# Kernel tuning notes

Hardware: AMD Instinct MI355X
Metric: run time of the kernel (lower is better)

## Reference

```python
import jax, jax.numpy as jnp
import numpy as np

N = 100000          # nodes
E = 3200000         # edges (before self-loops)
F_IN = 500          # Pubmed feature dim
H1, C1 = 8, 8       # layer-1 heads, channels per head
H2, C2 = 1, 7       # layer-2 heads, channels (num classes)
NEG_SLOPE = 0.2


def _glorot(key, shape, fan_in):
    return jax.random.normal(key, shape, dtype=jnp.float32) / np.sqrt(fan_in)


def setup_inputs() -> dict:
    key = jax.random.key(0)
    ks = jax.random.split(key, 10)
    x = jax.random.normal(ks[0], (N, F_IN), dtype=jnp.float32)
    edge_index = jax.random.randint(ks[1], (2, E), 0, N, dtype=jnp.int64)
    W1 = _glorot(ks[2], (F_IN, H1 * C1), F_IN)
    a_src1 = _glorot(ks[3], (H1, C1), C1)
    a_dst1 = _glorot(ks[4], (H1, C1), C1)
    b1 = jnp.zeros((H1 * C1,), dtype=jnp.float32)
    W2 = _glorot(ks[5], (H1 * C1, H2 * C2), H1 * C1)
    a_src2 = _glorot(ks[6], (H2, C2), C2)
    a_dst2 = _glorot(ks[7], (H2, C2), C2)
    b2 = jnp.zeros((H2 * C2,), dtype=jnp.float32)
    return {"x": x, "edge_index": edge_index, "W1": W1, "a_src1": a_src1,
            "a_dst1": a_dst1, "b1": b1, "W2": W2, "a_src2": a_src2,
            "a_dst2": a_dst2, "b2": b2}


def gat_conv(x, src, dst, W, a_src, a_dst, bias, heads, out_ch):
    # x: [N, F_in]; src/dst: [E'] (self-loops included); returns [N, heads*out_ch]
    h = (x @ W).reshape(N, heads, out_ch)                      # [N, H, C]
    alpha_s = jnp.einsum('nhc,hc->nh', h, a_src)               # [N, H]
    alpha_d = jnp.einsum('nhc,hc->nh', h, a_dst)               # [N, H]
    e = alpha_s[src] + alpha_d[dst]                            # [E', H]
    e = jax.nn.leaky_relu(e, NEG_SLOPE)
    # segment softmax over incoming edges of each dst node
    m = jax.ops.segment_max(e, dst, num_segments=N)            # [N, H]
    ex = jnp.exp(e - m[dst])                                   # [E', H]
    denom = jax.ops.segment_sum(ex, dst, num_segments=N)       # [N, H]
    alpha = ex / denom[dst]                                    # [E', H]
    msg = alpha[:, :, None] * h[src]                           # [E', H, C]
    out = jax.ops.segment_sum(msg, dst, num_segments=N)        # [N, H, C]
    return out.reshape(N, heads * out_ch) + bias


def reference(x, edge_index, W1, a_src1, a_dst1, b1, W2, a_src2, a_dst2, b2):
    loops = jnp.arange(N, dtype=edge_index.dtype)
    src = jnp.concatenate([edge_index[0], loops])
    dst = jnp.concatenate([edge_index[1], loops])
    h = gat_conv(x, src, dst, W1, a_src1, a_dst1, b1, H1, C1)   # [N, 64]
    out = gat_conv(h, src, dst, W2, a_src2, a_dst2, b2, H2, C2) # [N, 7]
    return jax.nn.log_softmax(out, axis=1)
```

## Files before the change

kernel.cpp:

```cpp
#include <hip/hip_runtime.h>
#include <hip/hip_bf16.h>
#include <hip/hip_fp16.h>

#define N_NODES 100000
#define N_EDGES 3200000
#define ET (N_EDGES + N_NODES)
#define F_IN 500
#define H1 8
#define C1 8
#define F1 64
#define C2 7

#define BSH 6
#define NB ((N_NODES + 63) / 64)
#define CAP2 4096
#define FB 128
#define FCHUNK ((ET + FB - 1) / FB)

typedef __attribute__((ext_vector_type(8))) short short8;
typedef __attribute__((ext_vector_type(4))) float f32x4;

__device__ __forceinline__ unsigned short f2bf(float f) {
    const unsigned u = __float_as_uint(f);
    return (unsigned short)((u + 0x7FFFu + ((u >> 16) & 1u)) >> 16);
}

__global__ __launch_bounds__(1024) void fill_count(const int* __restrict__ ei,
                                                   int* __restrict__ cntmat) {
    __shared__ int hist[NB];
    const int t = threadIdx.x, blk = blockIdx.x;
    for (int i = t; i < NB; i += 1024) hist[i] = 0;
    __syncthreads();
    const int s0 = blk * FCHUNK;
    const int s1 = min(s0 + FCHUNK, ET);
    for (int i = s0 + t; i < s1; i += 1024) {
        const int dst = (i < N_EDGES) ? ei[N_EDGES + i] : (i - N_EDGES);
        atomicAdd(&hist[dst >> BSH], 1);
    }
    __syncthreads();
    int* row = cntmat + (size_t)blk * NB;
    for (int i = t; i < NB; i += 1024) row[i] = hist[i];
}

__global__ __launch_bounds__(1024) void scan2a(const int* __restrict__ cntmat,
                                               int* __restrict__ boff,
                                               int* __restrict__ bexcl) {
    __shared__ int tot[2048];
    __shared__ int wsum[16];
    const int t = threadIdx.x;
    const int lane = t & 63;
    const int w = t >> 6;
    for (int b = t; b < 2048; b += 1024) {
        int s = 0;
        if (b < NB)
            for (int j = 0; j < FB; ++j) s += cntmat[(size_t)j * NB + b];
        tot[b] = s;
    }
    __syncthreads();
    int running = 0;
    for (int t0 = 0; t0 < 2048; t0 += 1024) {
        const int v = tot[t0 + t];
        int sc = v;
#pragma unroll
        for (int d = 1; d < 64; d <<= 1) {
            int u = __shfl_up(sc, d);
            if (lane >= d) sc += u;
        }
        if (lane == 63) wsum[w] = sc;
        __syncthreads();
        if (t < 16) {
            int ws = wsum[t];
#pragma unroll
            for (int d = 1; d < 16; d <<= 1) {
                int u = __shfl_up(ws, d);
                if (t >= d) ws += u;
            }
            wsum[t] = ws;
        }
        __syncthreads();
        const int excl = running + (w ? wsum[w - 1] : 0) + sc - v;
        if (t0 + t < NB) {
            boff[t0 + t] = excl;
            bexcl[t0 + t] = excl;
        }
        const int tt = wsum[15];
        __syncthreads();
        running += tt;
    }
    if (t == 0) boff[NB] = running;
}

__global__ __launch_bounds__(256) void scan2b(const int* __restrict__ cntmat,
                                              const int* __restrict__ bexcl,
                                              int* __restrict__ basemat) {
    const int b = blockIdx.x * 256 + threadIdx.x;
    if (b >= NB) return;
    int run = bexcl[b];
#pragma unroll 4
    for (int j = 0; j < FB; ++j) {
        basemat[(size_t)j * NB + b] = run;
        run += cntmat[(size_t)j * NB + b];
    }
}

__global__ __launch_bounds__(1024) void fill_scatter(const int* __restrict__ ei,
                                                     const int* __restrict__ basemat,
                                                     unsigned int* __restrict__ ebuf) {
    __shared__ int cur[NB];
    const int t = threadIdx.x, blk = blockIdx.x;
    const int* row = basemat + (size_t)blk * NB;
    for (int i = t; i < NB; i += 1024) cur[i] = row[i];
    __syncthreads();
    const int s0 = blk * FCHUNK;
    const int s1 = min(s0 + FCHUNK, ET);
    for (int i = s0 + t; i < s1; i += 1024) {
        int src, dst;
        if (i < N_EDGES) { src = ei[i]; dst = ei[N_EDGES + i]; }
        else             { src = dst = i - N_EDGES; }
        const int b = dst >> BSH;
        const int p = atomicAdd(&cur[b], 1);
        ebuf[p] = (unsigned)src | ((unsigned)(dst & 63) << 17);
    }
}

__global__ __launch_bounds__(256) void wprep(const float* __restrict__ W1,
                                             short* __restrict__ wpk) {
    const int idx = blockIdx.x * 256 + threadIdx.x;
    if (idx >= 32768) return;
    const int j = idx & 7;
    const int l = (idx >> 3) & 63;
    const int f = (idx >> 9) & 3;
    const int ks = idx >> 11;
    const int k = ks * 32 + ((l >> 4) << 3) + j;
    const int col = f * 16 + (l & 15);
    const float fv = (k < F_IN) ? W1[k * F1 + col] : 0.f;
    wpk[idx] = (short)f2bf(fv);
}

__global__ __launch_bounds__(256) void gemm1_kernel(
    const float* __restrict__ x, const short* __restrict__ wpk,
    const float* __restrict__ a_src, const float* __restrict__ a_dst,
    __half* __restrict__ h1, float* __restrict__ as1, float* __restrict__ ad1)
{
    const int t = threadIdx.x;
    const int l = t & 63;
    const int w = t >> 6;
    const int row0 = blockIdx.x * 64 + w * 16;
    const int r = l & 15;
    const int koff = (l >> 4) * 8;
    const float* __restrict__ xp =
        x + (size_t)min(row0 + r, N_NODES - 1) * F_IN + koff;
    const short* __restrict__ wl = wpk + (l << 3);

    f32x4 acc[4];
#pragma unroll
    for (int f = 0; f < 4; ++f) acc[f] = (f32x4){0.f, 0.f, 0.f, 0.f};

    float4 va = *(const float4*)(xp);
    float4 vb = *(const float4*)(xp + 4);
    short8 bcur[4];
#pragma unroll
    for (int f = 0; f < 4; ++f)
        bcur[f] = *(const short8*)(wl + (f << 9));

    for (int ks = 0; ks < 16; ++ks) {
        float v[8];
        v[0] = va.x; v[1] = va.y; v[2] = va.z; v[3] = va.w;
        v[4] = vb.x; v[5] = vb.y; v[6] = vb.z; v[7] = vb.w;
        if (ks < 14) {
            va = *(const float4*)(xp + (ks + 1) * 32);
            vb = *(const float4*)(xp + (ks + 1) * 32 + 4);
        } else if (ks == 14) {
            float tv[8];
#pragma unroll
            for (int j = 0; j < 8; ++j)
                tv[j] = (koff + j < 20) ? xp[480 + j] : 0.f;
            va = make_float4(tv[0], tv[1], tv[2], tv[3]);
            vb = make_float4(tv[4], tv[5], tv[6], tv[7]);
        }
        short8 bnext[4];
        if (ks < 15) {
#pragma unroll
            for (int f = 0; f < 4; ++f)
                bnext[f] = *(const short8*)(wl + (((ks + 1) * 4 + f) << 9));
        }
        short8 ah, al;
#pragma unroll
        for (int j = 0; j < 8; ++j) {
            const unsigned short h = f2bf(v[j]);
            ah[j] = (short)h;
            al[j] = (short)f2bf(v[j] - __uint_as_float((unsigned)h << 16));
        }
#pragma unroll
        for (int f = 0; f < 4; ++f) {
            acc[f] = __builtin_amdgcn_mfma_f32_16x16x32_bf16(ah, bcur[f], acc[f], 0, 0, 0);
            acc[f] = __builtin_amdgcn_mfma_f32_16x16x32_bf16(al, bcur[f], acc[f], 0, 0, 0);
        }
        if (ks < 15) {
#pragma unroll
            for (int f = 0; f < 4; ++f) bcur[f] = bnext[f];
        }
    }

    const int g = l >> 4;
    const int p = r >> 3;
    float asv[4], adv[4];
#pragma unroll
    for (int f = 0; f < 4; ++f) {
        asv[f] = a_src[f * 16 + r];
        adv[f] = a_dst[f * 16 + r];
    }
#pragma unroll
    for (int f = 0; f < 4; ++f) {
#pragma unroll
        for (int reg = 0; reg < 4; ++reg) {
            const int row = row0 + g * 4 + reg;
            const float hv = acc[f][reg];
            if (row < N_NODES)
                h1[(size_t)row * F1 + f * 16 + r] = __float2half(hv);
            float ps = hv * asv[f];
            float pd = hv * adv[f];
            ps += __shfl_xor(ps, 1); ps += __shfl_xor(ps, 2); ps += __shfl_xor(ps, 4);
            pd += __shfl_xor(pd, 1); pd += __shfl_xor(pd, 2); pd += __shfl_xor(pd, 4);
            if ((l & 7) == 0 && row < N_NODES) {
                as1[row * H1 + f * 2 + p] = ps;
                ad1[row * H1 + f * 2 + p] = pd;
            }
        }
    }
}

__global__ __launch_bounds__(256) void agg1_kernel(
    const int* __restrict__ boff, const unsigned int* __restrict__ ebuf,
    const __half* __restrict__ h1, const float* __restrict__ as1,
    const float* __restrict__ ad1, const float* __restrict__ b1,
    __half* __restrict__ hout, int* __restrict__ colidx,
    int* __restrict__ rowptrg)
{
    __shared__ int colb[CAP2];
    __shared__ int hist[64], curs[64], rowp[65];
    const int t = threadIdx.x, b = blockIdx.x;
    const int e0 = boff[b];
    const int cnt = boff[b + 1] - e0;
    const int l = t & 63;
    const int w = t >> 6;
    if (t < 64) hist[t] = 0;
    __syncthreads();

    if (cnt <= CAP2) {
        for (int i = t; i < cnt; i += 256)
            atomicAdd(&hist[ebuf[e0 + i] >> 17], 1);
        __syncthreads();
        if (t < 64) {
            const int v = hist[t];
            int sc = v;
#pragma unroll
            for (int d = 1; d < 64; d <<= 1) {
                int u = __shfl_up(sc, d);
                if (t >= d) sc += u;
            }
            rowp[t] = sc - v;
            curs[t] = sc - v;
            if (t == 63) rowp[64] = sc;
        }
        __syncthreads();
        for (int i = t; i < cnt; i += 256) {
            const unsigned v = ebuf[e0 + i];
            const int p = atomicAdd(&curs[v >> 17], 1);
            colb[p] = (int)(v & 0x1FFFFu);
        }
        __syncthreads();
        for (int i = t; i < cnt; i += 256) colidx[e0 + i] = colb[i];
        if (t < 65) rowptrg[b * 65 + t] = e0 + rowp[t];

        const int jsub = l & 7;
        const int hsub = l >> 3;
        const int pbase = l & 56;
        for (int ni = 0; ni < 16; ++ni) {
            const int d = w * 16 + ni;
            const int n = (b << 6) + d;
            if (n >= N_NODES) break;
            const int rr0 = rowp[d], rr1 = rowp[d + 1];
            const float adh = ad1[(n << 3) + hsub];
            float den = 0.f, acc = 0.f;
            int j0 = rr0;
            for (; j0 + 8 <= rr1; j0 += 8) {
                const int s_l = colb[j0 + jsub];
                float e = as1[(s_l << 3) + hsub] + adh;
                e = fmaxf(e, 0.2f * e);
                const float p_l = __expf(e);
#pragma unroll
                for (int j = 0; j < 8; ++j) {
                    const float p = __shfl(p_l, pbase + j);
                    const int s_j = __builtin_amdgcn_readlane(s_l, j);
                    const float v = __half2float(h1[((size_t)(unsigned)s_j << 6) + l]);
                    den += p;
                    acc = fmaf(p, v, acc);
                }
            }
            if (j0 < rr1) {
                const int s_l = colb[min(j0 + jsub, rr1 - 1)];
                float e = as1[(s_l << 3) + hsub] + adh;
                e = fmaxf(e, 0.2f * e);
                const float p_l = __expf(e);
#pragma unroll
                for (int j = 0; j < 8; ++j) {
                    if (j0 + j < rr1) {
                        const float p = __shfl(p_l, pbase + j);
                        const int s_j = __builtin_amdgcn_readlane(s_l, j);
                        const float v = __half2float(h1[((size_t)(unsigned)s_j << 6) + l]);
                        den += p;
                        acc = fmaf(p, v, acc);
                    }
                }
            }
            hout[((size_t)n << 6) + l] = __float2half(acc / den + b1[l]);
        }
    } else {
        const int hsub = l >> 3;
        for (int ni = 0; ni < 16; ++ni) {
            const int d = w * 16 + ni;
            const int n = (b << 6) + d;
            if (n >= N_NODES) break;
            const float adh = ad1[(n << 3) + hsub];
            float den = 0.f, acc = 0.f;
            for (int i = 0; i < cnt; ++i) {
                const unsigned v = ebuf[e0 + i];
                if ((int)(v >> 17) == d) {
                    const int s = (int)(v & 0x1FFFFu);
                    float e = as1[(s << 3) + hsub] + adh;
                    e = fmaxf(e, 0.2f * e);
                    const float p = __expf(e);
                    const float hv = __half2float(h1[((size_t)s << 6) + l]);
                    den += p;
                    acc = fmaf(p, hv, acc);
                }
            }
            hout[((size_t)n << 6) + l] = __float2half(acc / den + b1[l]);
        }
    }
}

__global__ __launch_bounds__(256) void gemm2_kernel(
    const __half* __restrict__ hin, const float* __restrict__ W2,
    const float* __restrict__ a_src, const float* __restrict__ a_dst,
    float* __restrict__ h2p, float* __restrict__ as2, float* __restrict__ ad2)
{
    __shared__ float w2s[F1 * C2];
    __shared__ float as_s[C2], ad_s[C2];
    for (int i = threadIdx.x; i < F1 * C2; i += blockDim.x) w2s[i] = W2[i];
    if (threadIdx.x < C2) { as_s[threadIdx.x] = a_src[threadIdx.x]; ad_s[threadIdx.x] = a_dst[threadIdx.x]; }
    __syncthreads();

    int n = blockIdx.x * blockDim.x + threadIdx.x;
    if (n >= N_NODES) return;
    float acc[C2];
#pragma unroll
    for (int c = 0; c < C2; ++c) acc[c] = 0.f;
    const short8* hp = (const short8*)(hin + ((size_t)n << 6));
#pragma unroll
    for (int k8 = 0; k8 < 8; ++k8) {
        const short8 h8 = hp[k8];
#pragma unroll
        for (int e = 0; e < 8; ++e) {
            const float hv = __half2float(__ushort_as_half((unsigned short)h8[e]));
            const int k = k8 * 8 + e;
#pragma unroll
            for (int c = 0; c < C2; ++c)
                acc[c] = fmaf(hv, w2s[k * C2 + c], acc[c]);
        }
    }
    float s = 0.f, d = 0.f;
#pragma unroll
    for (int c = 0; c < C2; ++c) {
        s = fmaf(acc[c], as_s[c], s);
        d = fmaf(acc[c], ad_s[c], d);
    }
    float4* o = (float4*)(h2p + (size_t)n * 8);
    o[0] = make_float4(acc[0], acc[1], acc[2], acc[3]);
    o[1] = make_float4(acc[4], acc[5], acc[6], 0.f);
    as2[n] = s;
    ad2[n] = d;
}

__global__ __launch_bounds__(256) void agg2_kernel(
    const int* __restrict__ boff, const unsigned int* __restrict__ ebuf,
    const int* __restrict__ rowptrg, const int* __restrict__ colidx,
    const float* __restrict__ h2p, const float* __restrict__ as2,
    const float* __restrict__ ad2, const float* __restrict__ b2,
    float* __restrict__ out)
{
    const int t = threadIdx.x, b = blockIdx.x;
    const int d = t >> 2;
    const int q = t & 3;
    const int n = (b << 6) + d;
    if (n >= N_NODES) return;
    const int cnt = boff[b + 1] - boff[b];
    const float adn = ad2[n];

    float denom = 0.f;
    float a0 = 0, a1 = 0, a2 = 0, a3 = 0, a4 = 0, a5 = 0, a6 = 0;
    if (cnt <= CAP2) {
        const int rr0 = rowptrg[b * 65 + d], rr1 = rowptrg[b * 65 + d + 1];
        for (int j = rr0 + q; j < rr1; j += 4) {
            const int s = colidx[j];
            float e = as2[s] + adn;
            e = fmaxf(e, 0.2f * e);
            const float ex = __expf(e);
            const float4 va = *(const float4*)(h2p + (size_t)s * 8);
            const float4 vb = *(const float4*)(h2p + (size_t)s * 8 + 4);
            denom += ex;
            a0 = fmaf(ex, va.x, a0); a1 = fmaf(ex, va.y, a1);
            a2 = fmaf(ex, va.z, a2); a3 = fmaf(ex, va.w, a3);
            a4 = fmaf(ex, vb.x, a4); a5 = fmaf(ex, vb.y, a5);
            a6 = fmaf(ex, vb.z, a6);
        }
    } else {
        const int e0 = boff[b];
        for (int i = q; i < cnt; i += 4) {
            const unsigned v = ebuf[e0 + i];
            if ((int)(v >> 17) == d) {
                const int s = (int)(v & 0x1FFFFu);
                float e = as2[s] + adn;
                e = fmaxf(e, 0.2f * e);
                const float ex = __expf(e);
                const float4 va = *(const float4*)(h2p + (size_t)s * 8);
                const float4 vb = *(const float4*)(h2p + (size_t)s * 8 + 4);
                denom += ex;
                a0 = fmaf(ex, va.x, a0); a1 = fmaf(ex, va.y, a1);
                a2 = fmaf(ex, va.z, a2); a3 = fmaf(ex, va.w, a3);
                a4 = fmaf(ex, vb.x, a4); a5 = fmaf(ex, vb.y, a5);
                a6 = fmaf(ex, vb.z, a6);
            }
        }
    }
#pragma unroll
    for (int dd = 1; dd < 4; dd <<= 1) {
        denom += __shfl_xor(denom, dd);
        a0 += __shfl_xor(a0, dd); a1 += __shfl_xor(a1, dd);
        a2 += __shfl_xor(a2, dd); a3 += __shfl_xor(a3, dd);
        a4 += __shfl_xor(a4, dd); a5 += __shfl_xor(a5, dd);
        a6 += __shfl_xor(a6, dd);
    }
    const float inv = 1.f / denom;
    float v0 = a0 * inv + b2[0], v1 = a1 * inv + b2[1];
    float v2 = a2 * inv + b2[2], v3 = a3 * inv + b2[3];
    float v4 = a4 * inv + b2[4], v5 = a5 * inv + b2[5];
    float v6 = a6 * inv + b2[6];
    float mx = fmaxf(fmaxf(fmaxf(v0, v1), fmaxf(v2, v3)), fmaxf(fmaxf(v4, v5), v6));
    const float se = __expf(v0 - mx) + __expf(v1 - mx) + __expf(v2 - mx) +
                     __expf(v3 - mx) + __expf(v4 - mx) + __expf(v5 - mx) +
                     __expf(v6 - mx);
    const float lse = __logf(se) + mx;
    const float wa = (q == 0) ? v0 : (q == 1) ? v1 : (q == 2) ? v2 : v3;
    const float wb = (q == 0) ? v4 : (q == 1) ? v5 : v6;
    out[n * C2 + q] = wa - lse;
    if (q < 3) out[n * C2 + q + 4] = wb - lse;
}

extern "C" void kernel_launch(void* const* d_in, const int* in_sizes, int n_in,
                              void* d_out, int out_size, void* d_ws, size_t ws_size,
                              hipStream_t stream) {
    const float* x      = (const float*)d_in[0];
    const int*   ei     = (const int*)  d_in[1];
    const float* W1     = (const float*)d_in[2];
    const float* a_src1 = (const float*)d_in[3];
    const float* a_dst1 = (const float*)d_in[4];
    const float* b1     = (const float*)d_in[5];
    const float* W2     = (const float*)d_in[6];
    const float* a_src2 = (const float*)d_in[7];
    const float* a_dst2 = (const float*)d_in[8];
    const float* b2     = (const float*)d_in[9];
    float* out = (float*)d_out;

    char* ws = (char*)d_ws;
    size_t off = 0;
    auto alloc = [&](size_t bytes) -> void* {
        void* p = ws + off;
        off += (bytes + 255) & ~(size_t)255;
        return p;
    };
    int*          boff    = (int*)   alloc((size_t)(NB + 1) * sizeof(int));
    int*          bexcl   = (int*)   alloc((size_t)NB * sizeof(int));
    int*          cntmat  = (int*)   alloc((size_t)FB * NB * sizeof(int));
    int*          basemat = (int*)   alloc((size_t)FB * NB * sizeof(int));
    unsigned int* ebuf    = (unsigned int*)alloc((size_t)ET * sizeof(unsigned int));
    int*          colidx  = (int*)   alloc((size_t)ET * sizeof(int));
    int*          rowptrg = (int*)   alloc((size_t)NB * 65 * sizeof(int));
    short*        wpk     = (short*) alloc((size_t)32768 * sizeof(short));
    __half*       h1      = (__half*)alloc((size_t)N_NODES * F1 * sizeof(__half));
    float*        as1     = (float*) alloc((size_t)N_NODES * H1 * sizeof(float));
    float*        ad1     = (float*) alloc((size_t)N_NODES * H1 * sizeof(float));
    __half*       hout1   = (__half*)alloc((size_t)N_NODES * F1 * sizeof(__half));
    float*        h2p     = (float*) alloc((size_t)N_NODES * 8 * sizeof(float));
    float*        as2     = (float*) alloc((size_t)N_NODES * sizeof(float));
    float*        ad2     = (float*) alloc((size_t)N_NODES * sizeof(float));

    wprep<<<128, 256, 0, stream>>>(W1, wpk);
    fill_count<<<FB, 1024, 0, stream>>>(ei, cntmat);
    scan2a<<<1, 1024, 0, stream>>>(cntmat, boff, bexcl);
    scan2b<<<(NB + 255) / 256, 256, 0, stream>>>(cntmat, bexcl, basemat);
    fill_scatter<<<FB, 1024, 0, stream>>>(ei, basemat, ebuf);
    gemm1_kernel<<<(N_NODES + 63) / 64, 256, 0, stream>>>(x, wpk, a_src1, a_dst1, h1, as1, ad1);
    agg1_kernel<<<NB, 256, 0, stream>>>(boff, ebuf, h1, as1, ad1, b1, hout1, colidx, rowptrg);
    gemm2_kernel<<<(N_NODES + 255) / 256, 256, 0, stream>>>(hout1, W2, a_src2, a_dst2, h2p, as2, ad2);
    agg2_kernel<<<NB, 256, 0, stream>>>(boff, ebuf, rowptrg, colidx, h2p, as2, ad2, b2, out);
}
```

Baseline: 345.9 us.

## Stage x tiles through swizzled double-buffered LDS in layer-1 GEMM

The layer-1 projection kernel now loads x cooperatively: 16 threads read each row in contiguous float4 segments, 64 columns at a time. The tiles go into a double-buffered, XOR-swizzled shared-memory buffer, and the MFMA lanes then read their fragments from it. This replaces each lane's short strided global reads with coalesced row reads, aimed at raising the effective bandwidth of the dominant 200MB x stream. The cost is a barrier per chunk and extra LDS traffic. Weight fragments are now loaded inline rather than prefetched in registers, and out-of-row padding reads are cancelled by the zero weights.

```diff
diff --git a/kernel.cpp b/kernel.cpp
--- a/kernel.cpp
+++ b/kernel.cpp
@@ -142,63 +142,78 @@
     const float* __restrict__ a_src, const float* __restrict__ a_dst,
     __half* __restrict__ h1, float* __restrict__ as1, float* __restrict__ ad1)
 {
+    __shared__ float xs[2][4096];
     const int t = threadIdx.x;
     const int l = t & 63;
     const int w = t >> 6;
-    const int row0 = blockIdx.x * 64 + w * 16;
-    const int r = l & 15;
-    const int koff = (l >> 4) * 8;
-    const float* __restrict__ xp =
-        x + (size_t)min(row0 + r, N_NODES - 1) * F_IN + koff;
+    const int row0 = blockIdx.x * 64;
+    const int srow = t >> 4;
+    const int sseg = t & 15;
+    const int r = l & 15, q = l >> 4;
+    const int myrow = w * 16 + r;
+    const int e = myrow & 7;
+    const int offA = myrow * 64 + (((q * 2) ^ e) << 2);
+    const int offB = myrow * 64 + ((((q * 2) | 1) ^ e) << 2);
     const short* __restrict__ wl = wpk + (l << 3);
+    const size_t maxidx = (size_t)N_NODES * F_IN - 4;
+
+    const int rg0 = min(row0 + srow, N_NODES - 1);
+    const int rg1 = min(row0 + 16 + srow, N_NODES - 1);
+    const int rg2 = min(row0 + 32 + srow, N_NODES - 1);
+    const int rg3 = min(row0 + 48 + srow, N_NODES - 1);
+    const int wseg0 = (sseg ^ (srow & 7)) << 2;
+    const int wseg1 = (sseg ^ ((16 + srow) & 7)) << 2;
+    const int wseg2 = (sseg ^ ((32 + srow) & 7)) << 2;
+    const int wseg3 = (sseg ^ ((48 + srow) & 7)) << 2;
 
     f32x4 acc[4];
 #pragma unroll
     for (int f = 0; f < 4; ++f) acc[f] = (f32x4){0.f, 0.f, 0.f, 0.f};
 
-    float4 va = *(const float4*)(xp);
-    float4 vb = *(const float4*)(xp + 4);
-    short8 bcur[4];
-#pragma unroll
-    for (int f = 0; f < 4; ++f)
-        bcur[f] = *(const short8*)(wl + (f << 9));
-
-    for (int ks = 0; ks < 16; ++ks) {
-        float v[8];
-        v[0] = va.x; v[1] = va.y; v[2] = va.z; v[3] = va.w;
-        v[4] = vb.x; v[5] = vb.y; v[6] = vb.z; v[7] = vb.w;
-        if (ks < 14) {
-            va = *(const float4*)(xp + (ks + 1) * 32);
-            vb = *(const float4*)(xp + (ks + 1) * 32 + 4);
-        } else if (ks == 14) {
-            float tv[8];
-#pragma unroll
-            for (int j = 0; j < 8; ++j)
-                tv[j] = (koff + j < 20) ? xp[480 + j] : 0.f;
-            va = make_float4(tv[0], tv[1], tv[2], tv[3]);
-            vb = make_float4(tv[4], tv[5], tv[6], tv[7]);
-        }
-        short8 bnext[4];
-        if (ks < 15) {
-#pragma unroll
-            for (int f = 0; f < 4; ++f)
-                bnext[f] = *(const short8*)(wl + (((ks + 1) * 4 + f) << 9));
-        }
-        short8 ah, al;
-#pragma unroll
-        for (int j = 0; j < 8; ++j) {
-            const unsigned short h = f2bf(v[j]);
-            ah[j] = (short)h;
-            al[j] = (short)f2bf(v[j] - __uint_as_float((unsigned)h << 16));
-        }
-#pragma unroll
-        for (int f = 0; f < 4; ++f) {
-            acc[f] = __builtin_amdgcn_mfma_f32_16x16x32_bf16(ah, bcur[f], acc[f], 0, 0, 0);
-            acc[f] = __builtin_amdgcn_mfma_f32_16x16x32_bf16(al, bcur[f], acc[f], 0, 0, 0);
-        }
-        if (ks < 15) {
-#pragma unroll
-            for (int f = 0; f < 4; ++f) bcur[f] = bnext[f];
+    float4 stg0, stg1, stg2, stg3;
+    {
+        const int k0 = 0;
+        stg0 = *(const float4*)(x + min((size_t)rg0 * F_IN + k0 + sseg * 4, maxidx));
+        stg1 = *(const float4*)(x + min((size_t)rg1 * F_IN + k0 + sseg * 4, maxidx));
+        stg2 = *(const float4*)(x + min((size_t)rg2 * F_IN + k0 + sseg * 4, maxidx));
+        stg3 = *(const float4*)(x + min((size_t)rg3 * F_IN + k0 + sseg * 4, maxidx));
+    }
+
+    for (int c = 0; c < 8; ++c) {
+        float* buf = xs[c & 1];
+        *(float4*)&buf[(srow)      * 64 + wseg0] = stg0;
+        *(float4*)&buf[(16 + srow) * 64 + wseg1] = stg1;
+        *(float4*)&buf[(32 + srow) * 64 + wseg2] = stg2;
+        *(float4*)&buf[(48 + srow) * 64 + wseg3] = stg3;
+        if (c < 7) {
+            const int k0 = (c + 1) * 64;
+            stg0 = *(const float4*)(x + min((size_t)rg0 * F_IN + k0 + sseg * 4, maxidx));
+            stg1 = *(const float4*)(x + min((size_t)rg1 * F_IN + k0 + sseg * 4, maxidx));
+            stg2 = *(const float4*)(x + min((size_t)rg2 * F_IN + k0 + sseg * 4, maxidx));
+            stg3 = *(const float4*)(x + min((size_t)rg3 * F_IN + k0 + sseg * 4, maxidx));
+        }
+        __syncthreads();
+#pragma unroll
+        for (int ksub = 0; ksub < 2; ++ksub) {
+            const float4 va = *(const float4*)&buf[offA + ksub * 32];
+            const float4 vb = *(const float4*)&buf[offB + ksub * 32];
+            float v[8];
+            v[0] = va.x; v[1] = va.y; v[2] = va.z; v[3] = va.w;
+            v[4] = vb.x; v[5] = vb.y; v[6] = vb.z; v[7] = vb.w;
+            short8 ah, al;
+#pragma unroll
+            for (int j = 0; j < 8; ++j) {
+                const unsigned short h = f2bf(v[j]);
+                ah[j] = (short)h;
+                al[j] = (short)f2bf(v[j] - __uint_as_float((unsigned)h << 16));
+            }
+            const int ks = c * 2 + ksub;
+#pragma unroll
+            for (int f = 0; f < 4; ++f) {
+                const short8 bh = *(const short8*)(wl + ((ks * 4 + f) << 9));
+                acc[f] = __builtin_amdgcn_mfma_f32_16x16x32_bf16(ah, bh, acc[f], 0, 0, 0);
+                acc[f] = __builtin_amdgcn_mfma_f32_16x16x32_bf16(al, bh, acc[f], 0, 0, 0);
+            }
         }
     }
 
@@ -214,7 +229,7 @@
     for (int f = 0; f < 4; ++f) {
 #pragma unroll
         for (int reg = 0; reg < 4; ++reg) {
-            const int row = row0 + g * 4 + reg;
+            const int row = row0 + w * 16 + g * 4 + reg;
             const float hv = acc[f][reg];
             if (row < N_NODES)
                 h1[(size_t)row * F1 + f * 16 + r] = __float2half(hv);
```

After: 351.7 us. About the same (+1.7%).
